# Performance work log

Hardware: AMD Instinct MI355X
Metric: run time of the kernel (lower is better)

## Reference

```python
import jax, jax.numpy as jnp
import numpy as np

B, T, E, H, L, V, CTX = 16, 1024, 512, 8, 6, 32, 1024
HD = E // H


def setup_inputs() -> dict:
    key = jax.random.key(0)
    ks = jax.random.split(key, 20)
    s = 0.02
    inp = {
        "tokens": jax.random.randint(ks[0], (B, T), 0, V),
        "emb": jax.random.normal(ks[1], (V, E), jnp.float32) * s,
        "pos_emb": jax.random.normal(ks[2], (CTX, E), jnp.float32) * s,
        "Wq": jax.random.normal(ks[3], (L, H, E, HD), jnp.float32) * s,
        "Wk": jax.random.normal(ks[4], (L, H, E, HD), jnp.float32) * s,
        "Wv": jax.random.normal(ks[5], (L, H, E, HD), jnp.float32) * s,
        "Wo": jax.random.normal(ks[6], (L, E, E), jnp.float32) * s,
        "bo": jnp.zeros((L, E), jnp.float32),
        "ln1_g": jnp.ones((L, E), jnp.float32),
        "ln1_b": jnp.zeros((L, E), jnp.float32),
        "ln2_g": jnp.ones((L, E), jnp.float32),
        "ln2_b": jnp.zeros((L, E), jnp.float32),
        "W1": jax.random.normal(ks[7], (L, E, E), jnp.float32) * s,
        "b1": jnp.zeros((L, E), jnp.float32),
        "W2": jax.random.normal(ks[8], (L, E, E), jnp.float32) * s,
        "b2": jnp.zeros((L, E), jnp.float32),
        "lnf_g": jnp.ones((E,), jnp.float32),
        "lnf_b": jnp.zeros((E,), jnp.float32),
        "Wf": jax.random.normal(ks[9], (E, V), jnp.float32) * s,
        "bf": jnp.zeros((V,), jnp.float32),
    }
    return inp


def _layernorm(x, g, b, eps=1e-5):
    mu = x.mean(-1, keepdims=True)
    var = ((x - mu) ** 2).mean(-1, keepdims=True)
    return (x - mu) * jax.lax.rsqrt(var + eps) * g + b


def reference(tokens, emb, pos_emb, Wq, Wk, Wv, Wo, bo, ln1_g, ln1_b,
              ln2_g, ln2_b, W1, b1, W2, b2, lnf_g, lnf_b, Wf, bf):
    Bt, Tt = tokens.shape
    x = emb[tokens] + pos_emb[:Tt]  # [B,T,E]
    causal = jnp.tril(jnp.ones((Tt, Tt), bool))

    def block(x, p):
        wq, wk, wv, wo, bo_, g1, b1_, g2, b2_, w1, bb1, w2, bb2 = p
        h = _layernorm(x, g1, b1_)
        q = jnp.einsum('bte,hed->bhtd', h, wq)
        k = jnp.einsum('bte,hed->bhtd', h, wk)
        v = jnp.einsum('bte,hed->bhtd', h, wv)
        # NOTE: source applies NO 1/sqrt(d) scaling
        s = jnp.einsum('bhtd,bhsd->bhts', q, k)
        s = jnp.where(causal, s, -jnp.inf)
        a = jax.nn.softmax(s, axis=-1)
        o = jnp.einsum('bhts,bhsd->bhtd', a, v)
        o = o.transpose(0, 2, 1, 3).reshape(Bt, Tt, E)  # concat heads
        x = x + jnp.einsum('bte,ef->btf', o, wo) + bo_
        h2 = _layernorm(x, g2, b2_)
        f = jax.nn.relu(jnp.einsum('bte,ef->btf', h2, w1) + bb1)
        f = jnp.einsum('bte,ef->btf', f, w2) + bb2
        return x + f, None

    x, _ = jax.lax.scan(block, x, (Wq, Wk, Wv, Wo, bo, ln1_g, ln1_b,
                                   ln2_g, ln2_b, W1, b1, W2, b2))
    x = _layernorm(x, lnf_g, lnf_b)
    logits = jnp.einsum('bte,ev->btv', x, Wf) + bf
    return logits
```

## Files before the change

### kernel.cpp

```cpp
#include <hip/hip_runtime.h>
#include <hip/hip_bf16.h>

namespace {

constexpr int B = 16, T = 1024, E = 512, H = 8, L = 6, V = 32, HD = 64;
constexpr int BT = B * T;
constexpr long S = (long)BT * E;
constexpr int QS = 1536;

typedef __attribute__((ext_vector_type(8))) short bf16x8;
typedef __attribute__((ext_vector_type(4))) float f32x4;

__device__ inline float b2f(ushort u) {
  union { unsigned u; float f; } v; v.u = (unsigned)u << 16; return v.f;
}
__device__ inline ushort f2b(float f) {
  union { float f; unsigned u; } v; v.f = f;
  unsigned r = v.u + 0x7FFFu + ((v.u >> 16) & 1u);
  return (ushort)(r >> 16);
}
__device__ inline void gl_lds16(const ushort* g, ushort* lds) {
  __builtin_amdgcn_global_load_lds(
      (const __attribute__((address_space(1))) void*)g,
      (__attribute__((address_space(3))) void*)lds, 16, 0, 0);
}

__global__ void embed_kernel(const int* __restrict__ tokens,
                             const float* __restrict__ emb,
                             const float* __restrict__ pos,
                             float* __restrict__ x) {
  int idx = blockIdx.x * blockDim.x + threadIdx.x;
  constexpr int TOT = BT * (E / 4);
  if (idx >= TOT) return;
  int row = idx >> 7, c4 = idx & 127;
  int t = row & (T - 1);
  int tok = tokens[row];
  float4 a = reinterpret_cast<const float4*>(emb + (long)tok * E)[c4];
  float4 p = reinterpret_cast<const float4*>(pos + (long)t * E)[c4];
  float4 r;
  r.x = a.x + p.x; r.y = a.y + p.y; r.z = a.z + p.z; r.w = a.w + p.w;
  reinterpret_cast<float4*>(x + (long)row * E)[c4] = r;
}

__global__ __launch_bounds__(256)
void wconv_kernel(const float* __restrict__ in, ushort* __restrict__ out,
                  int K, int Nn, int ppl, long layer_stride, long off) {
  const int z = blockIdx.z;
  const long pin = (long)z * K * Nn;
  const long pout = (long)(z / ppl) * layer_stride + off +
                    (long)(z % ppl) * Nn * K;
  __shared__ float t[32][33];
  const int k0 = blockIdx.x * 32, n0 = blockIdx.y * 32;
  const int tid = threadIdx.x, r = tid >> 5, c = tid & 31;
  #pragma unroll
  for (int i = 0; i < 4; i++)
    t[r + i * 8][c] = in[pin + (long)(k0 + r + i * 8) * Nn + n0 + c];
  __syncthreads();
  #pragma unroll
  for (int i = 0; i < 4; i++)
    out[pout + (long)(n0 + r + i * 8) * K + k0 + c] = f2b(t[c][r + i * 8]);
}

__global__ __launch_bounds__(128)
void ln_kernel(const float* __restrict__ x, const float* __restrict__ g,
               const float* __restrict__ b, ushort* __restrict__ out) {
  int row = blockIdx.x, tid = threadIdx.x;
  float4 v = reinterpret_cast<const float4*>(x + (long)row * E)[tid];
  float s = v.x + v.y + v.z + v.w;
  #pragma unroll
  for (int off = 32; off > 0; off >>= 1) s += __shfl_down(s, off, 64);
  __shared__ float r1[2], r2[2];
  int lane = tid & 63, wid = tid >> 6;
  if (lane == 0) r1[wid] = s;
  __syncthreads();
  float mean = (r1[0] + r1[1]) * (1.0f / E);
  float4 d;
  d.x = v.x - mean; d.y = v.y - mean; d.z = v.z - mean; d.w = v.w - mean;
  float s2 = d.x * d.x + d.y * d.y + d.z * d.z + d.w * d.w;
  #pragma unroll
  for (int off = 32; off > 0; off >>= 1) s2 += __shfl_down(s2, off, 64);
  if (lane == 0) r2[wid] = s2;
  __syncthreads();
  float rstd = rsqrtf((r2[0] + r2[1]) * (1.0f / E) + 1e-5f);
  float4 gg = reinterpret_cast<const float4*>(g)[tid];
  float4 bb = reinterpret_cast<const float4*>(b)[tid];
  ushort4 o;
  o.x = f2b(d.x * rstd * gg.x + bb.x);
  o.y = f2b(d.y * rstd * gg.y + bb.y);
  o.z = f2b(d.z * rstd * gg.z + bb.z);
  o.w = f2b(d.w * rstd * gg.w + bb.w);
  reinterpret_cast<ushort4*>(out + (long)row * E)[tid] = o;
}

template <int MODE>
__global__ __launch_bounds__(256, 2)
void bgemm_kernel(const ushort* __restrict__ A, const ushort* __restrict__ Bt,
                  const float* __restrict__ bias, const float* __restrict__ res,
                  void* __restrict__ Cout, int Nl) {
  constexpr int K = 512;
  __shared__ ushort As[128][32];
  __shared__ ushort Bs[128][32];
  const int tid = threadIdx.x, lane = tid & 63, wid = tid >> 6;
  const int bm = blockIdx.x * 128, bn = blockIdx.y * 128;
  const int wm = (wid >> 1) * 64, wn = (wid & 1) * 64;
  const int lo = lane & 15, hi = lane >> 4;
  const int arow = lane >> 2, acol = (lane & 3) * 8;
  f32x4 acc[4][4] = {};
  for (int k0 = 0; k0 < K; k0 += 32) {
    #pragma unroll
    for (int i = 0; i < 2; i++) {
      int seg = wid * 2 + i;
      gl_lds16(A + (long)(bm + seg * 16 + arow) * K + k0 + acol,
               &As[seg * 16][0]);
      gl_lds16(Bt + (long)(bn + seg * 16 + arow) * K + k0 + acol,
               &Bs[seg * 16][0]);
    }
    __syncthreads();
    bf16x8 af[4], bfr[4];
    #pragma unroll
    for (int mi = 0; mi < 4; mi++)
      af[mi] = *(const bf16x8*)&As[wm + mi * 16 + lo][hi * 8];
    #pragma unroll
    for (int ni = 0; ni < 4; ni++)
      bfr[ni] = *(const bf16x8*)&Bs[wn + ni * 16 + lo][hi * 8];
    #pragma unroll
    for (int mi = 0; mi < 4; mi++)
      #pragma unroll
      for (int ni = 0; ni < 4; ni++)
        acc[mi][ni] = __builtin_amdgcn_mfma_f32_16x16x32_bf16(
            af[mi], bfr[ni], acc[mi][ni], 0, 0, 0);
    __syncthreads();
  }
  #pragma unroll
  for (int mi = 0; mi < 4; mi++) {
    #pragma unroll
    for (int ni = 0; ni < 4; ni++) {
      const int gn = bn + wn + ni * 16 + lo;
      const float bv = (MODE >= 1) ? bias[gn] : 0.f;
      #pragma unroll
      for (int r = 0; r < 4; r++) {
        const long gm = bm + wm + mi * 16 + hi * 4 + r;
        float vv = acc[mi][ni][r];
        if (MODE == 0) {
          ((ushort*)Cout)[gm * Nl + gn] = f2b(vv);
        } else if (MODE == 1) {
          ((float*)Cout)[gm * Nl + gn] = vv + bv + res[gm * Nl + gn];
        } else {
          ((ushort*)Cout)[gm * Nl + gn] = f2b(fmaxf(vv + bv, 0.f));
        }
      }
    }
  }
}

__global__ __launch_bounds__(256, 2)
void attn_kernel(const ushort* __restrict__ qkv, ushort* __restrict__ o) {
  const int b = blockIdx.z, h = blockIdx.y;
  const int qt = (gridDim.x - 1) - blockIdx.x;
  const int tid = threadIdx.x, wid = tid >> 6, lane = tid & 63;
  const int lo = lane & 15, hi = lane >> 4;
  const long bh = (long)b * T;
  const int qbase = qt * 128 + wid * 32;
  const int dch = qt * 2 + (wid >> 1);
  const int roff = 32 * (wid & 1);
  __shared__ ushort Ks[2][64 * 64];
  __shared__ ushort Vs[2][64 * 64];
  __shared__ ushort Ps[4][32 * 64];
  char* PsB = (char*)Ps[wid];

  bf16x8 qf[2][2];
  #pragma unroll
  for (int mf = 0; mf < 2; mf++)
    #pragma unroll
    for (int kh = 0; kh < 2; kh++)
      qf[mf][kh] = *(const bf16x8*)(qkv + (bh + qbase + mf * 16 + lo) * QS +
                                    h * 64 + kh * 32 + hi * 8);
  f32x4 accO[2][4] = {};
  float m[2][4], lsum[2][4];
  #pragma unroll
  for (int a = 0; a < 2; a++)
    #pragma unroll
    for (int r = 0; r < 4; r++) { m[a][r] = -1e30f; lsum[a][r] = 0.f; }

  const ushort* kb = qkv + bh * QS + 512 + h * 64;
  const ushort* vb = qkv + bh * QS + 1024 + h * 64;
  const int nch = qt * 2 + 2;

  uint4 kpre[2], vpre[2];
  const int kkey0 = tid >> 3, kc8 = tid & 7;
  const int vkey0 = (tid & 31) * 2, vdim0 = (tid >> 5) * 8;
  auto LOADC = [&](int cc) {
    const long s0 = (long)cc * 64;
    kpre[0] = *(const uint4*)(kb + (s0 + kkey0) * QS + kc8 * 8);
    kpre[1] = *(const uint4*)(kb + (s0 + kkey0 + 32) * QS + kc8 * 8);
    vpre[0] = *(const uint4*)(vb + (s0 + vkey0) * QS + vdim0);
    vpre[1] = *(const uint4*)(vb + (s0 + vkey0 + 1) * QS + vdim0);
  };
  auto WRITEC = [&](int buf) {
    char* KsB = (char*)Ks[buf];
    char* VsB = (char*)Vs[buf];
    #pragma unroll
    for (int it = 0; it < 2; it++) {
      const int key = kkey0 + it * 32;
      *(uint4*)(KsB + ((key * 128 + kc8 * 16) ^ ((key & 7) << 4))) = kpre[it];
    }
    const ushort* p0 = (const ushort*)&vpre[0];
    const ushort* p1 = (const ushort*)&vpre[1];
    #pragma unroll
    for (int j = 0; j < 8; j++) {
      const int dim = vdim0 + j;
      ushort2 w; w.x = p0[j]; w.y = p1[j];
      *(ushort2*)(VsB + ((dim * 128 + vkey0 * 2) ^ ((dim & 7) << 4))) = w;
    }
  };

  LOADC(0);
  WRITEC(0);
  __syncthreads();

  for (int c = 0; c < nch; c++) {
    const int cur = c & 1;
    if (c + 1 < nch) LOADC(c + 1);
    if (c <= dch) {
      char* KsB = (char*)Ks[cur];
      char* VsB = (char*)Vs[cur];
      const bool diag = (c == dch);
      bf16x8 kf[4][2];
      #pragma unroll
      for (int nf = 0; nf < 4; nf++)
        #pragma unroll
        for (int kh = 0; kh < 2; kh++) {
          const int key = nf * 16 + lo;
          kf[nf][kh] = *(const bf16x8*)(
              KsB + ((key * 128 + kh * 64 + hi * 16) ^ ((key & 7) << 4)));
        }
      #pragma unroll
      for (int mf = 0; mf < 2; mf++) {
        f32x4 s[4];
        __builtin_amdgcn_s_setprio(1);
        #pragma unroll
        for (int nf = 0; nf < 4; nf++) {
          f32x4 z = {0.f, 0.f, 0.f, 0.f};
          z = __builtin_amdgcn_mfma_f32_16x16x32_bf16(qf[mf][0], kf[nf][0],
                                                      z, 0, 0, 0);
          z = __builtin_amdgcn_mfma_f32_16x16x32_bf16(qf[mf][1], kf[nf][1],
                                                      z, 0, 0, 0);
          s[nf] = z;
        }
        __builtin_amdgcn_s_setprio(0);
        if (diag) {
          #pragma unroll
          for (int nf = 0; nf < 4; nf++)
            #pragma unroll
            for (int r = 0; r < 4; r++)
              if (nf * 16 + lo > roff + mf * 16 + hi * 4 + r)
                s[nf][r] = -1e30f;
        }
        #pragma unroll
        for (int r = 0; r < 4; r++) {
          float pm = fmaxf(fmaxf(s[0][r], s[1][r]), fmaxf(s[2][r], s[3][r]));
          #pragma unroll
          for (int msk = 1; msk < 16; msk <<= 1)
            pm = fmaxf(pm, __shfl_xor(pm, msk, 64));
          const float mn = fmaxf(m[mf][r], pm);
          const float sc = __expf(m[mf][r] - mn);
          m[mf][r] = mn;
          float p0 = __expf(s[0][r] - mn), p1 = __expf(s[1][r] - mn);
          float p2 = __expf(s[2][r] - mn), p3 = __expf(s[3][r] - mn);
          lsum[mf][r] = lsum[mf][r] * sc + (p0 + p1 + p2 + p3);
          #pragma unroll
          for (int nd = 0; nd < 4; nd++) accO[mf][nd][r] *= sc;
          const int ql = mf * 16 + hi * 4 + r;
          const int swz = (ql & 7) << 4;
          *(ushort*)(PsB + ((ql * 128 + (lo) * 2) ^ swz))      = f2b(p0);
          *(ushort*)(PsB + ((ql * 128 + (16 + lo) * 2) ^ swz)) = f2b(p1);
          *(ushort*)(PsB + ((ql * 128 + (32 + lo) * 2) ^ swz)) = f2b(p2);
          *(ushort*)(PsB + ((ql * 128 + (48 + lo) * 2) ^ swz)) = f2b(p3);
        }
      }
      asm volatile("s_waitcnt lgkmcnt(0)" ::: "memory");
      #pragma unroll
      for (int ks = 0; ks < 2; ks++) {
        bf16x8 pa[2];
        #pragma unroll
        for (int mf = 0; mf < 2; mf++) {
          const int ql = mf * 16 + lo;
          pa[mf] = *(const bf16x8*)(
              PsB + ((ql * 128 + ks * 64 + hi * 16) ^ ((ql & 7) << 4)));
        }
        __builtin_amdgcn_s_setprio(1);
        #pragma unroll
        for (int nd = 0; nd < 4; nd++) {
          const int dim = nd * 16 + lo;
          bf16x8 vf = *(const bf16x8*)(
              VsB + ((dim * 128 + ks * 64 + hi * 16) ^ ((dim & 7) << 4)));
          #pragma unroll
          for (int mf = 0; mf < 2; mf++)
            accO[mf][nd] = __builtin_amdgcn_mfma_f32_16x16x32_bf16(
                pa[mf], vf, accO[mf][nd], 0, 0, 0);
        }
        __builtin_amdgcn_s_setprio(0);
      }
    }
    if (c + 1 < nch) WRITEC(cur ^ 1);
    __syncthreads();
  }
  #pragma unroll
  for (int mf = 0; mf < 2; mf++)
    #pragma unroll
    for (int r = 0; r < 4; r++) {
      float l = lsum[mf][r];
      #pragma unroll
      for (int msk = 1; msk < 16; msk <<= 1) l += __shfl_xor(l, msk, 64);
      lsum[mf][r] = 1.0f / l;
    }
  #pragma unroll
  for (int mf = 0; mf < 2; mf++)
    #pragma unroll
    for (int nd = 0; nd < 4; nd++)
      #pragma unroll
      for (int r = 0; r < 4; r++) {
        const int ql = mf * 16 + hi * 4 + r, dim = nd * 16 + lo;
        *(ushort*)(PsB + ql * 128 + dim * 2) =
            f2b(accO[mf][nd][r] * lsum[mf][r]);
      }
  asm volatile("s_waitcnt lgkmcnt(0)" ::: "memory");
  #pragma unroll
  for (int it = 0; it < 4; it++) {
    const int idx = it * 64 + lane;
    const int row = idx >> 3, c8 = idx & 7;
    uint4 val = *(const uint4*)(PsB + row * 128 + c8 * 16);
    *(uint4*)(o + (bh + qbase + row) * E + h * 64 + c8 * 8) = val;
  }
}

__global__ __launch_bounds__(256)
void logits_kernel(const ushort* __restrict__ xf, const ushort* __restrict__ WfT,
                   const float* __restrict__ bf, float* __restrict__ out) {
  __shared__ float xs[8][E];
  const int row0 = blockIdx.x * 8, tid = threadIdx.x;
  #pragma unroll
  for (int i = 0; i < 4; i++) {
    int idx = i * 256 + tid;
    int r = idx >> 7, c4 = idx & 127;
    ushort4 u = ((const ushort4*)(xf + (long)(row0 + r) * E))[c4];
    float4 f;
    f.x = b2f(u.x); f.y = b2f(u.y); f.z = b2f(u.z); f.w = b2f(u.w);
    *(float4*)&xs[r][c4 * 4] = f;
  }
  __syncthreads();
  const int r = tid >> 5, c = tid & 31;
  float acc = 0.f;
  for (int e8 = 0; e8 < 64; e8++) {
    uint4 w = *(const uint4*)(WfT + (long)c * E + e8 * 8);
    const ushort* ws = (const ushort*)&w;
    #pragma unroll
    for (int j = 0; j < 8; j++) acc += xs[r][e8 * 8 + j] * b2f(ws[j]);
  }
  out[(long)(row0 + r) * V + c] = acc + bf[c];
}

}

extern "C" void kernel_launch(void* const* d_in, const int* in_sizes, int n_in,
                              void* d_out, int out_size, void* d_ws,
                              size_t ws_size, hipStream_t stream) {
  const int*   tokens = (const int*)d_in[0];
  const float* emb    = (const float*)d_in[1];
  const float* pos    = (const float*)d_in[2];
  const float* Wq     = (const float*)d_in[3];
  const float* Wk     = (const float*)d_in[4];
  const float* Wv     = (const float*)d_in[5];
  const float* Wo     = (const float*)d_in[6];
  const float* bo     = (const float*)d_in[7];
  const float* ln1g   = (const float*)d_in[8];
  const float* ln1b   = (const float*)d_in[9];
  const float* ln2g   = (const float*)d_in[10];
  const float* ln2b   = (const float*)d_in[11];
  const float* W1     = (const float*)d_in[12];
  const float* b1     = (const float*)d_in[13];
  const float* W2     = (const float*)d_in[14];
  const float* b2     = (const float*)d_in[15];
  const float* lnfg   = (const float*)d_in[16];
  const float* lnfb   = (const float*)d_in[17];
  const float* Wf     = (const float*)d_in[18];
  const float* bf     = (const float*)d_in[19];
  float* out = (float*)d_out;

  char* p = (char*)d_ws;
  float*  x    = (float*)p;          p += S * 4;
  ushort* hb   = (ushort*)p;         p += S * 2;
  ushort* qkvb = (ushort*)p;         p += (long)BT * QS * 2;
  const long WSZ = (long)L * E * E;
  ushort* wqkvT = (ushort*)p;        p += (long)L * QS * E * 2;
  ushort* woT  = (ushort*)p;         p += WSZ * 2;
  ushort* w1T  = (ushort*)p;         p += WSZ * 2;
  ushort* w2T  = (ushort*)p;         p += WSZ * 2;
  ushort* wfT  = (ushort*)p;         p += (long)E * V * 2;

  const long QLS = (long)QS * E;

  wconv_kernel<<<dim3(16, 2, L * H), 256, 0, stream>>>(Wq, wqkvT, E, HD, H,
                                                       QLS, 0);
  wconv_kernel<<<dim3(16, 2, L * H), 256, 0, stream>>>(Wk, wqkvT, E, HD, H,
                                                       QLS, (long)512 * E);
  wconv_kernel<<<dim3(16, 2, L * H), 256, 0, stream>>>(Wv, wqkvT, E, HD, H,
                                                       QLS, (long)1024 * E);
  wconv_kernel<<<dim3(16, 16, L), 256, 0, stream>>>(Wo, woT, E, E, 1,
                                                    (long)E * E, 0);
  wconv_kernel<<<dim3(16, 16, L), 256, 0, stream>>>(W1, w1T, E, E, 1,
                                                    (long)E * E, 0);
  wconv_kernel<<<dim3(16, 16, L), 256, 0, stream>>>(W2, w2T, E, E, 1,
                                                    (long)E * E, 0);
  wconv_kernel<<<dim3(16, 1, 1), 256, 0, stream>>>(Wf, wfT, E, V, 1,
                                                   (long)E * V, 0);

  embed_kernel<<<(BT * (E / 4) + 255) / 256, 256, 0, stream>>>(tokens, emb,
                                                               pos, x);

  const dim3 gq(BT / 128, QS / 128);
  const dim3 gg(BT / 128, E / 128);
  const dim3 ga(T / 128, H, B);

  for (int l = 0; l < L; l++) {
    const long wo = (long)l * E * E;
    ln_kernel<<<BT, 128, 0, stream>>>(x, ln1g + l * E, ln1b + l * E, hb);
    bgemm_kernel<0><<<gq, 256, 0, stream>>>(hb, wqkvT + l * QLS, nullptr,
                                            nullptr, qkvb, QS);
    attn_kernel<<<ga, 256, 0, stream>>>(qkvb, hb);
    bgemm_kernel<1><<<gg, 256, 0, stream>>>(hb, woT + wo, bo + l * E, x, x,
                                            E);
    ln_kernel<<<BT, 128, 0, stream>>>(x, ln2g + l * E, ln2b + l * E, hb);
    bgemm_kernel<2><<<gg, 256, 0, stream>>>(hb, w1T + wo, b1 + l * E, nullptr,
                                            qkvb, E);
    bgemm_kernel<1><<<gg, 256, 0, stream>>>((ushort*)qkvb, w2T + wo,
                                            b2 + l * E, x, x, E);
  }

  ln_kernel<<<BT, 128, 0, stream>>>(x, lnfg, lnfb, hb);
  logits_kernel<<<BT / 8, 256, 0, stream>>>(hb, wfT, bf, out);
}
```

Measured before the change: 1.557 ms.

## Split attention key range across two blocks and merge partial softmax results

Each 128-row query tile is now handled by two blocks, each covering half of the causal key chunks. Each block writes an unnormalized bf16 partial output plus per-row max and sum. A new merge kernel rescales and combines the two halves into the final head output. The aim is to double the number of blocks and even out the triangular causal workload across CUs. In exchange, the K/V double-buffered prefetch is replaced by a single-buffered synchronous load, the wave-priority hints are dropped, occupancy is raised to 4 blocks per CU, and an extra kernel launch plus a round trip of partials through global memory is added.

Measured after the change: 2.659 ms. +70.8%, slower.

```diff
diff --git a/kernel.cpp b/kernel.cpp
--- a/kernel.cpp
+++ b/kernel.cpp
@@ -153,19 +153,24 @@
   }
 }
 
-__global__ __launch_bounds__(256, 2)
-void attn_kernel(const ushort* __restrict__ qkv, ushort* __restrict__ o) {
+__global__ __launch_bounds__(256, 4)
+void attn_kernel(const ushort* __restrict__ qkv, ushort* __restrict__ Op,
+                 float* __restrict__ ml) {
   const int b = blockIdx.z, h = blockIdx.y;
-  const int qt = (gridDim.x - 1) - blockIdx.x;
+  const int qt = 7 - (blockIdx.x >> 1);
+  const int half = blockIdx.x & 1;
   const int tid = threadIdx.x, wid = tid >> 6, lane = tid & 63;
   const int lo = lane & 15, hi = lane >> 4;
   const long bh = (long)b * T;
   const int qbase = qt * 128 + wid * 32;
   const int dch = qt * 2 + (wid >> 1);
   const int roff = 32 * (wid & 1);
-  __shared__ ushort Ks[2][64 * 64];
-  __shared__ ushort Vs[2][64 * 64];
+  const int clo = half * (qt + 1), chi = clo + (qt + 1);
+  __shared__ ushort Ks[64 * 64];
+  __shared__ ushort Vs[64 * 64];
   __shared__ ushort Ps[4][32 * 64];
+  char* KsB = (char*)Ks;
+  char* VsB = (char*)Vs;
   char* PsB = (char*)Ps[wid];
 
   bf16x8 qf[2][2];
@@ -184,46 +189,31 @@
 
   const ushort* kb = qkv + bh * QS + 512 + h * 64;
   const ushort* vb = qkv + bh * QS + 1024 + h * 64;
-  const int nch = qt * 2 + 2;
-
-  uint4 kpre[2], vpre[2];
-  const int kkey0 = tid >> 3, kc8 = tid & 7;
-  const int vkey0 = (tid & 31) * 2, vdim0 = (tid >> 5) * 8;
-  auto LOADC = [&](int cc) {
-    const long s0 = (long)cc * 64;
-    kpre[0] = *(const uint4*)(kb + (s0 + kkey0) * QS + kc8 * 8);
-    kpre[1] = *(const uint4*)(kb + (s0 + kkey0 + 32) * QS + kc8 * 8);
-    vpre[0] = *(const uint4*)(vb + (s0 + vkey0) * QS + vdim0);
-    vpre[1] = *(const uint4*)(vb + (s0 + vkey0 + 1) * QS + vdim0);
-  };
-  auto WRITEC = [&](int buf) {
-    char* KsB = (char*)Ks[buf];
-    char* VsB = (char*)Vs[buf];
+
+  for (int c = clo; c < chi; c++) {
+    const long s0 = (long)c * 64;
     #pragma unroll
     for (int it = 0; it < 2; it++) {
-      const int key = kkey0 + it * 32;
-      *(uint4*)(KsB + ((key * 128 + kc8 * 16) ^ ((key & 7) << 4))) = kpre[it];
-    }
-    const ushort* p0 = (const ushort*)&vpre[0];
-    const ushort* p1 = (const ushort*)&vpre[1];
-    #pragma unroll
-    for (int j = 0; j < 8; j++) {
-      const int dim = vdim0 + j;
-      ushort2 w; w.x = p0[j]; w.y = p1[j];
-      *(ushort2*)(VsB + ((dim * 128 + vkey0 * 2) ^ ((dim & 7) << 4))) = w;
-    }
-  };
-
-  LOADC(0);
-  WRITEC(0);
-  __syncthreads();
-
-  for (int c = 0; c < nch; c++) {
-    const int cur = c & 1;
-    if (c + 1 < nch) LOADC(c + 1);
+      int idx = it * 256 + tid;
+      int key = idx >> 3, c8 = idx & 7;
+      uint4 kv = *(const uint4*)(kb + (s0 + key) * QS + c8 * 8);
+      *(uint4*)(KsB + ((key * 128 + c8 * 16) ^ ((key & 7) << 4))) = kv;
+    }
+    {
+      const int key0 = (tid & 31) * 2, dim0 = (tid >> 5) * 8;
+      uint4 v0 = *(const uint4*)(vb + (s0 + key0) * QS + dim0);
+      uint4 v1 = *(const uint4*)(vb + (s0 + key0 + 1) * QS + dim0);
+      const ushort* p0 = (const ushort*)&v0;
+      const ushort* p1 = (const ushort*)&v1;
+      #pragma unroll
+      for (int j = 0; j < 8; j++) {
+        const int dim = dim0 + j;
+        ushort2 w; w.x = p0[j]; w.y = p1[j];
+        *(ushort2*)(VsB + ((dim * 128 + key0 * 2) ^ ((dim & 7) << 4))) = w;
+      }
+    }
+    __syncthreads();
     if (c <= dch) {
-      char* KsB = (char*)Ks[cur];
-      char* VsB = (char*)Vs[cur];
       const bool diag = (c == dch);
       bf16x8 kf[4][2];
       #pragma unroll
@@ -237,7 +227,6 @@
       #pragma unroll
       for (int mf = 0; mf < 2; mf++) {
         f32x4 s[4];
-        __builtin_amdgcn_s_setprio(1);
         #pragma unroll
         for (int nf = 0; nf < 4; nf++) {
           f32x4 z = {0.f, 0.f, 0.f, 0.f};
@@ -247,7 +236,6 @@
                                                       z, 0, 0, 0);
           s[nf] = z;
         }
-        __builtin_amdgcn_s_setprio(0);
         if (diag) {
           #pragma unroll
           for (int nf = 0; nf < 4; nf++)
@@ -288,7 +276,6 @@
           pa[mf] = *(const bf16x8*)(
               PsB + ((ql * 128 + ks * 64 + hi * 16) ^ ((ql & 7) << 4)));
         }
-        __builtin_amdgcn_s_setprio(1);
         #pragma unroll
         for (int nd = 0; nd < 4; nd++) {
           const int dim = nd * 16 + lo;
@@ -299,10 +286,8 @@
             accO[mf][nd] = __builtin_amdgcn_mfma_f32_16x16x32_bf16(
                 pa[mf], vf, accO[mf][nd], 0, 0, 0);
         }
-        __builtin_amdgcn_s_setprio(0);
-      }
-    }
-    if (c + 1 < nch) WRITEC(cur ^ 1);
+      }
+    }
     __syncthreads();
   }
   #pragma unroll
@@ -312,8 +297,19 @@
       float l = lsum[mf][r];
       #pragma unroll
       for (int msk = 1; msk < 16; msk <<= 1) l += __shfl_xor(l, msk, 64);
-      lsum[mf][r] = 1.0f / l;
-    }
+      lsum[mf][r] = l;
+    }
+  const long tile = ((long)(b * H + h) * 8 + qt) * 2 + half;
+  if (lo == 0) {
+    #pragma unroll
+    for (int mf = 0; mf < 2; mf++)
+      #pragma unroll
+      for (int r = 0; r < 4; r++) {
+        const int row = wid * 32 + mf * 16 + hi * 4 + r;
+        ml[(tile * 128 + row) * 2 + 0] = m[mf][r];
+        ml[(tile * 128 + row) * 2 + 1] = lsum[mf][r];
+      }
+  }
   #pragma unroll
   for (int mf = 0; mf < 2; mf++)
     #pragma unroll
@@ -321,16 +317,46 @@
       #pragma unroll
       for (int r = 0; r < 4; r++) {
         const int ql = mf * 16 + hi * 4 + r, dim = nd * 16 + lo;
-        *(ushort*)(PsB + ql * 128 + dim * 2) =
-            f2b(accO[mf][nd][r] * lsum[mf][r]);
+        *(ushort*)(PsB + ql * 128 + dim * 2) = f2b(accO[mf][nd][r]);
       }
   asm volatile("s_waitcnt lgkmcnt(0)" ::: "memory");
+  ushort* obase = Op + (tile * 128 + wid * 32) * 64;
   #pragma unroll
   for (int it = 0; it < 4; it++) {
     const int idx = it * 64 + lane;
     const int row = idx >> 3, c8 = idx & 7;
     uint4 val = *(const uint4*)(PsB + row * 128 + c8 * 16);
-    *(uint4*)(o + (bh + qbase + row) * E + h * 64 + c8 * 8) = val;
+    *(uint4*)(obase + row * 64 + c8 * 8) = val;
+  }
+}
+
+__global__ __launch_bounds__(256)
+void amerge_kernel(const ushort* __restrict__ Op, const float* __restrict__ ml,
+                   ushort* __restrict__ o) {
+  const int qt = blockIdx.x, h = blockIdx.y, b = blockIdx.z;
+  const int row = threadIdx.x >> 1, seg = threadIdx.x & 1;
+  const long t0 = ((long)(b * H + h) * 8 + qt) * 2;
+  const float m0 = ml[(t0 * 128 + row) * 2], l0 = ml[(t0 * 128 + row) * 2 + 1];
+  const float m1 = ml[((t0 + 1) * 128 + row) * 2],
+              l1 = ml[((t0 + 1) * 128 + row) * 2 + 1];
+  const float M = fmaxf(m0, m1);
+  float w0 = __expf(m0 - M), w1 = __expf(m1 - M);
+  const float inv = 1.0f / (l0 * w0 + l1 * w1);
+  w0 *= inv; w1 *= inv;
+  const ushort* p0 = Op + (t0 * 128 + row) * 64 + seg * 32;
+  const ushort* p1 = Op + ((t0 + 1) * 128 + row) * 64 + seg * 32;
+  ushort* orow = o + ((long)(b * T + qt * 128 + row)) * E + h * 64 + seg * 32;
+  #pragma unroll
+  for (int i = 0; i < 4; i++) {
+    uint4 a = ((const uint4*)p0)[i];
+    uint4 c = ((const uint4*)p1)[i];
+    const ushort* pa = (const ushort*)&a;
+    const ushort* pc = (const ushort*)&c;
+    ushort rr[8];
+    #pragma unroll
+    for (int j = 0; j < 8; j++)
+      rr[j] = f2b(b2f(pa[j]) * w0 + b2f(pc[j]) * w1);
+    ((uint4*)orow)[i] = *(const uint4*)rr;
   }
 }
 
@@ -397,6 +423,8 @@
   ushort* w1T  = (ushort*)p;         p += WSZ * 2;
   ushort* w2T  = (ushort*)p;         p += WSZ * 2;
   ushort* wfT  = (ushort*)p;         p += (long)E * V * 2;
+  ushort* aOp  = (ushort*)p;         p += (long)2048 * 128 * 64 * 2;
+  float*  aml  = (float*)p;          p += (long)2048 * 128 * 2 * 4;
 
   const long QLS = (long)QS * E;
 
@@ -420,14 +448,16 @@
 
   const dim3 gq(BT / 128, QS / 128);
   const dim3 gg(BT / 128, E / 128);
-  const dim3 ga(T / 128, H, B);
+  const dim3 ga(16, H, B);
+  const dim3 gm(8, H, B);
 
   for (int l = 0; l < L; l++) {
     const long wo = (long)l * E * E;
     ln_kernel<<<BT, 128, 0, stream>>>(x, ln1g + l * E, ln1b + l * E, hb);
     bgemm_kernel<0><<<gq, 256, 0, stream>>>(hb, wqkvT + l * QLS, nullptr,
                                             nullptr, qkvb, QS);
-    attn_kernel<<<ga, 256, 0, stream>>>(qkvb, hb);
+    attn_kernel<<<ga, 256, 0, stream>>>(qkvb, aOp, aml);
+    amerge_kernel<<<gm, 256, 0, stream>>>(aOp, aml, hb);
     bgemm_kernel<1><<<gg, 256, 0, stream>>>(hb, woT + wo, bo + l * E, x, x,
                                             E);
     ln_kernel<<<BT, 128, 0, stream>>>(x, ln2g + l * E, ln2b + l * E, hb);
```

## Drop attention K/V double buffering and raise occupancy bounds

Applied to the files above, without the earlier changes.

Replaces the register-prefetched, double-buffered K/V staging in the attention kernel with a single LDS buffer that is loaded and synced at the start of each chunk. It also removes the s_setprio hints and raises the launch_bounds minimum blocks per CU (GEMM to 3, attention to 4). The goal is to cut LDS and register pressure so more waves stay resident and hide latency through occupancy rather than software pipelining. In exchange, global loads are no longer overlapped with compute inside a block, and the tighter register caps may cause spills.

Measured after the change: 2.483 ms. 59.4% more time.

```diff
diff --git a/kernel.cpp b/kernel.cpp
--- a/kernel.cpp
+++ b/kernel.cpp
@@ -93,7 +93,7 @@
 }
 
 template <int MODE>
-__global__ __launch_bounds__(256, 2)
+__global__ __launch_bounds__(256, 3)
 void bgemm_kernel(const ushort* __restrict__ A, const ushort* __restrict__ Bt,
                   const float* __restrict__ bias, const float* __restrict__ res,
                   void* __restrict__ Cout, int Nl) {
@@ -153,7 +153,7 @@
   }
 }
 
-__global__ __launch_bounds__(256, 2)
+__global__ __launch_bounds__(256, 4)
 void attn_kernel(const ushort* __restrict__ qkv, ushort* __restrict__ o) {
   const int b = blockIdx.z, h = blockIdx.y;
   const int qt = (gridDim.x - 1) - blockIdx.x;
@@ -163,9 +163,11 @@
   const int qbase = qt * 128 + wid * 32;
   const int dch = qt * 2 + (wid >> 1);
   const int roff = 32 * (wid & 1);
-  __shared__ ushort Ks[2][64 * 64];
-  __shared__ ushort Vs[2][64 * 64];
+  __shared__ ushort Ks[64 * 64];
+  __shared__ ushort Vs[64 * 64];
   __shared__ ushort Ps[4][32 * 64];
+  char* KsB = (char*)Ks;
+  char* VsB = (char*)Vs;
   char* PsB = (char*)Ps[wid];
 
   bf16x8 qf[2][2];
@@ -186,44 +188,30 @@
   const ushort* vb = qkv + bh * QS + 1024 + h * 64;
   const int nch = qt * 2 + 2;
 
-  uint4 kpre[2], vpre[2];
-  const int kkey0 = tid >> 3, kc8 = tid & 7;
-  const int vkey0 = (tid & 31) * 2, vdim0 = (tid >> 5) * 8;
-  auto LOADC = [&](int cc) {
-    const long s0 = (long)cc * 64;
-    kpre[0] = *(const uint4*)(kb + (s0 + kkey0) * QS + kc8 * 8);
-    kpre[1] = *(const uint4*)(kb + (s0 + kkey0 + 32) * QS + kc8 * 8);
-    vpre[0] = *(const uint4*)(vb + (s0 + vkey0) * QS + vdim0);
-    vpre[1] = *(const uint4*)(vb + (s0 + vkey0 + 1) * QS + vdim0);
-  };
-  auto WRITEC = [&](int buf) {
-    char* KsB = (char*)Ks[buf];
-    char* VsB = (char*)Vs[buf];
+  for (int c = 0; c < nch; c++) {
+    const long s0 = (long)c * 64;
     #pragma unroll
     for (int it = 0; it < 2; it++) {
-      const int key = kkey0 + it * 32;
-      *(uint4*)(KsB + ((key * 128 + kc8 * 16) ^ ((key & 7) << 4))) = kpre[it];
-    }
-    const ushort* p0 = (const ushort*)&vpre[0];
-    const ushort* p1 = (const ushort*)&vpre[1];
-    #pragma unroll
-    for (int j = 0; j < 8; j++) {
-      const int dim = vdim0 + j;
-      ushort2 w; w.x = p0[j]; w.y = p1[j];
-      *(ushort2*)(VsB + ((dim * 128 + vkey0 * 2) ^ ((dim & 7) << 4))) = w;
-    }
-  };
-
-  LOADC(0);
-  WRITEC(0);
-  __syncthreads();
-
-  for (int c = 0; c < nch; c++) {
-    const int cur = c & 1;
-    if (c + 1 < nch) LOADC(c + 1);
+      int idx = it * 256 + tid;
+      int key = idx >> 3, c8 = idx & 7;
+      uint4 kv = *(const uint4*)(kb + (s0 + key) * QS + c8 * 8);
+      *(uint4*)(KsB + ((key * 128 + c8 * 16) ^ ((key & 7) << 4))) = kv;
+    }
+    {
+      const int key0 = (tid & 31) * 2, dim0 = (tid >> 5) * 8;
+      uint4 v0 = *(const uint4*)(vb + (s0 + key0) * QS + dim0);
+      uint4 v1 = *(const uint4*)(vb + (s0 + key0 + 1) * QS + dim0);
+      const ushort* p0 = (const ushort*)&v0;
+      const ushort* p1 = (const ushort*)&v1;
+      #pragma unroll
+      for (int j = 0; j < 8; j++) {
+        const int dim = dim0 + j;
+        ushort2 w; w.x = p0[j]; w.y = p1[j];
+        *(ushort2*)(VsB + ((dim * 128 + key0 * 2) ^ ((dim & 7) << 4))) = w;
+      }
+    }
+    __syncthreads();
     if (c <= dch) {
-      char* KsB = (char*)Ks[cur];
-      char* VsB = (char*)Vs[cur];
       const bool diag = (c == dch);
       bf16x8 kf[4][2];
       #pragma unroll
@@ -237,7 +225,6 @@
       #pragma unroll
       for (int mf = 0; mf < 2; mf++) {
         f32x4 s[4];
-        __builtin_amdgcn_s_setprio(1);
         #pragma unroll
         for (int nf = 0; nf < 4; nf++) {
           f32x4 z = {0.f, 0.f, 0.f, 0.f};
@@ -247,7 +234,6 @@
                                                       z, 0, 0, 0);
           s[nf] = z;
         }
-        __builtin_amdgcn_s_setprio(0);
         if (diag) {
           #pragma unroll
           for (int nf = 0; nf < 4; nf++)
@@ -288,7 +274,6 @@
           pa[mf] = *(const bf16x8*)(
               PsB + ((ql * 128 + ks * 64 + hi * 16) ^ ((ql & 7) << 4)));
         }
-        __builtin_amdgcn_s_setprio(1);
         #pragma unroll
         for (int nd = 0; nd < 4; nd++) {
           const int dim = nd * 16 + lo;
@@ -299,10 +284,8 @@
             accO[mf][nd] = __builtin_amdgcn_mfma_f32_16x16x32_bf16(
                 pa[mf], vf, accO[mf][nd], 0, 0, 0);
         }
-        __builtin_amdgcn_s_setprio(0);
       }
     }
-    if (c + 1 < nch) WRITEC(cur ^ 1);
     __syncthreads();
   }
   #pragma unroll
```
